# Kernel optimization log

Measured on AMD Instinct MI355X. Metric: run time of the kernel, lower is better.

The kernel has to match this reference:

```python
import jax, jax.numpy as jnp
import numpy as np

N_NODES = 8192
N_EDGES = 262144
D_IN = 512
D_OUT = 512


def setup_inputs() -> dict:
    key = jax.random.key(0)
    k1, k2, k3 = jax.random.split(key, 3)
    x = jax.random.normal(k1, (N_NODES, D_IN), dtype=jnp.float32)
    edge_index = jax.random.randint(k2, (2, N_EDGES), 0, N_NODES, dtype=jnp.int64)
    weight = jax.random.normal(k3, (D_IN, D_OUT), dtype=jnp.float32)
    bias = jnp.zeros((D_OUT,), dtype=jnp.float32)
    return {"x": x, "edge_index": edge_index, "weight": weight, "bias": bias}


def reference(x, edge_index, weight, bias):
    # GCN layer with selfloop=True branch of the original module.
    n = x.shape[0]
    # Dense symmetric adjacency via scatter-set, matching adj[ei0,ei1]=1; adj[ei1,ei0]=1
    adj = jnp.zeros((n, n), dtype=x.dtype)
    adj = adj.at[edge_index[0], edge_index[1]].set(1.0)
    adj = adj.at[edge_index[1], edge_index[0]].set(1.0)
    # Add self loops, symmetric degree normalization D^{-1/2} A D^{-1/2}
    adj = adj + jnp.eye(n, dtype=x.dtype)
    deg = jnp.sum(adj, axis=1)
    dinv = 1.0 / jnp.sqrt(deg)
    adj = adj * dinv[:, None] * dinv[None, :]  # == D @ adj @ D (diagonal scaling)
    return adj @ (x @ weight) + bias
```

## Files before the change

kernel.cpp:

```cpp
#include <hip/hip_runtime.h>
#include <hip/hip_bf16.h>


#define ELL_STRIDE 128

typedef __attribute__((ext_vector_type(8))) short bf16x8;
typedef __attribute__((ext_vector_type(4))) float f32x4;

__device__ __forceinline__ unsigned short f2bf(float f) {
  unsigned u = __float_as_uint(f);
  u = (u + 0x7fff + ((u >> 16) & 1)) >> 16;
  return (unsigned short)u;
}
__device__ __forceinline__ float bflo(unsigned u) {
  return __uint_as_float(u << 16);
}
__device__ __forceinline__ float bfhi(unsigned u) {
  return __uint_as_float(u & 0xffff0000u);
}

__global__ __launch_bounds__(256) void fused_front_kernel(
    const int* __restrict__ ei, unsigned* __restrict__ mask, int n_edges,
    int words,
    const float* __restrict__ x, unsigned short* __restrict__ xb, int n4,
    const float* __restrict__ W, unsigned short* __restrict__ Wt, int K, int N,
    unsigned short* __restrict__ Hs, int n_nodes,
    int edge_blocks, int cast_blocks, int tr_blocks) {
  const int bid = blockIdx.x;
  if (bid < edge_blocks) {
    const int e = bid * 256 + threadIdx.x;
    if (e < n_edges) {
      const int u = ei[e];
      const int v = ei[e + n_edges];
      atomicOr(&mask[(size_t)u * words + (v >> 5)], 1u << (v & 31));
      atomicOr(&mask[(size_t)v * words + (u >> 5)], 1u << (u & 31));
    }
    return;
  }
  if (bid < edge_blocks + cast_blocks) {
    const int t = (bid - edge_blocks) * 256 + threadIdx.x;
    if (t < n4) {
      float4 v = ((const float4*)x)[t];
      ushort4 o;
      o.x = f2bf(v.x); o.y = f2bf(v.y); o.z = f2bf(v.z); o.w = f2bf(v.w);
      ((ushort4*)xb)[t] = o;
    }
    return;
  }
  if (bid < edge_blocks + cast_blocks + tr_blocks) {
    __shared__ float tile[32][33];
    const int b = bid - edge_blocks - cast_blocks;
    const int bx = b & ((N >> 5) - 1);
    const int by = b >> (31 - __builtin_clz(N >> 5));
    const int tx = threadIdx.x & 31;
    const int ty = threadIdx.x >> 5;
#pragma unroll
    for (int r = 0; r < 4; ++r)
      tile[ty + 8 * r][tx] = W[(size_t)(by * 32 + ty + 8 * r) * N + bx * 32 + tx];
    __syncthreads();
#pragma unroll
    for (int r = 0; r < 4; ++r)
      Wt[(size_t)(bx * 32 + ty + 8 * r) * K + by * 32 + tx] =
          f2bf(tile[tx][ty + 8 * r]);
    return;
  }
  {
    const int t = threadIdx.x;
    if (t < (N >> 1)) ((unsigned*)(Hs + (size_t)n_nodes * N))[t] = 0;
  }
}

__global__ __launch_bounds__(256) void fused_mid_kernel(
    const unsigned short* __restrict__ xb,
    const unsigned short* __restrict__ Wt,
    unsigned short* __restrict__ Hs,
    const unsigned* __restrict__ mask, unsigned short* __restrict__ ell,
    int* __restrict__ deg, float* __restrict__ dinv,
    int M, int N, int K, int words, int gemm_blocks, int nbx_sh) {
  __shared__ unsigned short As[256 * 8];
  __shared__ unsigned short Bs[256 * 8];

  const int tid = threadIdx.x;
  const int bid = blockIdx.x;

  if (bid < gemm_blocks) {
    if (bid == 0 && tid == 0) dinv[M] = 0.f;
    const int wave = tid >> 6;
    const int lane = tid & 63;
    const int q = lane >> 4;
    const int c = lane & 15;
    const int bx = bid & ((1 << nbx_sh) - 1);
    const int by = bid >> nbx_sh;
    const int m0 = by * 64;
    const int n0 = bx * 64;
    const int wr = wave >> 1, wc = wave & 1;

    f32x4 acc[2][2] = {};

    for (int k0 = 0; k0 < K; k0 += 32) {
      {
        const unsigned short* g =
            xb + (size_t)(m0 + lane) * K + k0 + wave * 8;
        __builtin_amdgcn_global_load_lds(
            (const __attribute__((address_space(1))) void*)g,
            (__attribute__((address_space(3))) void*)(As + wave * 64 * 8), 16, 0, 0);
      }
      {
        const int s = tid;
        const unsigned short* g =
            Wt + (size_t)(n0 + (s >> 2)) * K + k0 + (s & 3) * 8;
        __builtin_amdgcn_global_load_lds(
            (const __attribute__((address_space(1))) void*)g,
            (__attribute__((address_space(3))) void*)(Bs + wave * 64 * 8), 16, 0, 0);
      }
      __syncthreads();

      bf16x8 a[2], b[2];
#pragma unroll
      for (int tm = 0; tm < 2; ++tm) {
        const int row = wr * 32 + tm * 16 + c;
        a[tm] = *(const bf16x8*)(As + (q * 64 + row) * 8);
      }
#pragma unroll
      for (int tn = 0; tn < 2; ++tn) {
        const int n = wc * 32 + tn * 16 + c;
        b[tn] = *(const bf16x8*)(Bs + (n * 4 + q) * 8);
      }
#pragma unroll
      for (int tm = 0; tm < 2; ++tm)
#pragma unroll
        for (int tn = 0; tn < 2; ++tn)
          acc[tm][tn] = __builtin_amdgcn_mfma_f32_16x16x32_bf16(
              a[tm], b[tn], acc[tm][tn], 0, 0, 0);
      __syncthreads();
    }

#pragma unroll
    for (int tm = 0; tm < 2; ++tm) {
#pragma unroll
      for (int r = 0; r < 4; ++r) {
        const int grow = m0 + wr * 32 + tm * 16 + q * 4 + r;
#pragma unroll
        for (int tn = 0; tn < 2; ++tn) {
          const int gcol = n0 + wc * 32 + tn * 16 + c;
          Hs[(size_t)grow * N + gcol] = f2bf(acc[tm][tn][r]);
        }
      }
    }
    return;
  }

  {
    const int wave = tid >> 6, lane = tid & 63;
    const int node = (bid - gemm_blocks) * 4 + wave;
    const unsigned* __restrict__ row = mask + (size_t)node * words;
    unsigned short* __restrict__ out = ell + (size_t)node * ELL_STRIDE;

    int running = 0;
    for (int r = 0; r < words; r += 64) {
      const int w = r + lane;
      unsigned bits = row[w];
      const int cnt = __popc(bits);
      int x = cnt;
#pragma unroll
      for (int d = 1; d < 64; d <<= 1) {
        int y = __shfl_up(x, d, 64);
        if (lane >= d) x += y;
      }
      int pos = running + x - cnt;
      while (bits) {
        const int b = __builtin_ctz(bits);
        bits &= bits - 1;
        if (pos < ELL_STRIDE) out[pos] = (unsigned short)((w << 5) + b);
        ++pos;
      }
      running += __shfl(x, 63, 64);
    }
    if (lane == 0) {
      const int dd = running < ELL_STRIDE ? running : ELL_STRIDE;
      deg[node] = dd;
      dinv[node] = rsqrtf((float)running + 1.0f);
      if (running < ELL_STRIDE) out[running] = (unsigned short)M;
      if (running + 1 < ELL_STRIDE) out[running + 1] = (unsigned short)M;
    }
  }
}

__global__ __launch_bounds__(256) void spmm_kernel(
    const unsigned short* __restrict__ ell, const int* __restrict__ deg,
    const float* __restrict__ dinv, const unsigned short* __restrict__ Hs,
    const float* __restrict__ bias, float* __restrict__ out, int n, int D) {
  __shared__ unsigned short jl[4][ELL_STRIDE];
  const int wave = threadIdx.x >> 6, lane = threadIdx.x & 63;
  const int i = blockIdx.x * 4 + wave;
  const int h = blockIdx.y;
  const int side = lane >> 5, hl = lane & 31;
  const int Dh = D >> 1;

  jl[wave][lane] = ell[(size_t)i * ELL_STRIDE + lane];
  jl[wave][64 + lane] = ell[(size_t)i * ELL_STRIDE + 64 + lane];
  const int d = deg[i];
  const float di = dinv[i];
  const int kmax = (d + 1) & ~1;

  const unsigned short* __restrict__ hb = Hs + h * Dh + hl * 8;
  float acc[8] = {0.f, 0.f, 0.f, 0.f, 0.f, 0.f, 0.f, 0.f};

  {
    const int js = side ? n : i;
    const float ds = side ? 0.f : di;
    const uint4 hv = *(const uint4*)(hb + (size_t)js * D);
    acc[0] += ds * bflo(hv.x); acc[1] += ds * bfhi(hv.x);
    acc[2] += ds * bflo(hv.y); acc[3] += ds * bfhi(hv.y);
    acc[4] += ds * bflo(hv.z); acc[5] += ds * bfhi(hv.z);
    acc[6] += ds * bflo(hv.w); acc[7] += ds * bfhi(hv.w);
  }
#pragma unroll 8
  for (int k = 0; k < kmax; k += 2) {
    const int j = jl[wave][k + side];
    const float dj = dinv[j];
    const uint4 hv = *(const uint4*)(hb + (size_t)j * D);
    acc[0] += dj * bflo(hv.x); acc[1] += dj * bfhi(hv.x);
    acc[2] += dj * bflo(hv.y); acc[3] += dj * bfhi(hv.y);
    acc[4] += dj * bflo(hv.z); acc[5] += dj * bfhi(hv.z);
    acc[6] += dj * bflo(hv.w); acc[7] += dj * bfhi(hv.w);
  }
#pragma unroll
  for (int t = 0; t < 8; ++t) acc[t] += __shfl_xor(acc[t], 32, 64);

  if (side == 0) {
    const float4 b0 = *(const float4*)(bias + h * Dh + hl * 8);
    const float4 b1 = *(const float4*)(bias + h * Dh + hl * 8 + 4);
    float* op = out + (size_t)i * D + h * Dh + hl * 8;
    float4 o0, o1;
    o0.x = di * acc[0] + b0.x; o0.y = di * acc[1] + b0.y;
    o0.z = di * acc[2] + b0.z; o0.w = di * acc[3] + b0.w;
    o1.x = di * acc[4] + b1.x; o1.y = di * acc[5] + b1.y;
    o1.z = di * acc[6] + b1.z; o1.w = di * acc[7] + b1.w;
    *(float4*)op = o0;
    *(float4*)(op + 4) = o1;
  }
}

extern "C" void kernel_launch(void* const* d_in, const int* in_sizes, int n_in,
                              void* d_out, int out_size, void* d_ws, size_t ws_size,
                              hipStream_t stream) {
  const float* x    = (const float*)d_in[0];
  const int*   ei   = (const int*)d_in[1];
  const float* W    = (const float*)d_in[2];
  const float* bias = (const float*)d_in[3];
  float* out = (float*)d_out;

  const int d_out_dim = in_sizes[3];
  const int d_in_dim  = in_sizes[2] / d_out_dim;
  const int n_nodes   = in_sizes[0] / d_in_dim;
  const int n_edges   = in_sizes[1] / 2;
  const int words     = (n_nodes + 31) / 32;

  char* ws = (char*)d_ws;
  size_t off = 0;
  unsigned* mask = (unsigned*)(ws + off); off += (size_t)n_nodes * words * 4;
  int* deg       = (int*)(ws + off);      off += (size_t)n_nodes * 4;
  float* dinv    = (float*)(ws + off);    off += (size_t)(n_nodes + 1) * 4;
  unsigned short* ell = (unsigned short*)(ws + off); off += (size_t)n_nodes * ELL_STRIDE * 2;
  unsigned short* xb  = (unsigned short*)(ws + off); off += (size_t)n_nodes * d_in_dim * 2;
  unsigned short* Wt  = (unsigned short*)(ws + off); off += (size_t)d_in_dim * d_out_dim * 2;
  unsigned short* Hs  = (unsigned short*)(ws + off);
  off += (size_t)(n_nodes + 1) * d_out_dim * 2;

  hipMemsetAsync(mask, 0, (size_t)n_nodes * words * 4, stream);

  const int edge_blocks = (n_edges + 255) / 256;
  const int n4 = n_nodes * d_in_dim / 4;
  const int cast_blocks = (n4 + 255) / 256;
  const int tr_blocks = (d_in_dim / 32) * (d_out_dim / 32);
  fused_front_kernel<<<edge_blocks + cast_blocks + tr_blocks + 1, 256, 0, stream>>>(
      ei, mask, n_edges, words, x, xb, n4, W, Wt, d_in_dim, d_out_dim,
      Hs, n_nodes, edge_blocks, cast_blocks, tr_blocks);

  const int nbx = d_out_dim / 64;
  const int nbx_sh = 31 - __builtin_clz(nbx);
  const int gemm_blocks = nbx * (n_nodes / 64);
  const int ell_blocks = n_nodes / 4;
  fused_mid_kernel<<<gemm_blocks + ell_blocks, 256, 0, stream>>>(
      xb, Wt, Hs, mask, ell, deg, dinv,
      n_nodes, d_out_dim, d_in_dim, words, gemm_blocks, nbx_sh);

  dim3 sgrid(n_nodes / 4, 2);
  spmm_kernel<<<sgrid, 256, 0, stream>>>(ell, deg, dinv, Hs, bias, out,
                                         n_nodes, d_out_dim);
}
```

Before: 161.0 us.

## Double GEMM K-step, fold self-loop into ELL, prefetch dinv into LDS

The GEMM loop now stages 64 K-elements per iteration instead of 32, so it runs half as many barrier pairs per tile, at the cost of twice the LDS footprint. The ELL builder writes the node itself as the self-loop entry and pads the rest of the row with the sentinel index. This removes the separate self-loop load in the SpMM. The SpMM also gathers dinv for every neighbour once into shared memory alongside the index, which takes the dependent global dinv load out of the inner loop. Zeroing of dinv[n] moves to the front kernel so the ELL and SpMM stages see it.

Measured after the change: 157.7 us (median of 2 runs). 2.0% less time.

```diff
diff --git a/kernel.cpp b/kernel.cpp
--- a/kernel.cpp
+++ b/kernel.cpp
@@ -24,7 +24,7 @@
     int words,
     const float* __restrict__ x, unsigned short* __restrict__ xb, int n4,
     const float* __restrict__ W, unsigned short* __restrict__ Wt, int K, int N,
-    unsigned short* __restrict__ Hs, int n_nodes,
+    unsigned short* __restrict__ Hs, float* __restrict__ dinv, int n_nodes,
     int edge_blocks, int cast_blocks, int tr_blocks) {
   const int bid = blockIdx.x;
   if (bid < edge_blocks) {
@@ -67,6 +67,7 @@
   {
     const int t = threadIdx.x;
     if (t < (N >> 1)) ((unsigned*)(Hs + (size_t)n_nodes * N))[t] = 0;
+    if (t == 0) dinv[n_nodes] = 0.f;
   }
 }
 
@@ -77,14 +78,13 @@
     const unsigned* __restrict__ mask, unsigned short* __restrict__ ell,
     int* __restrict__ deg, float* __restrict__ dinv,
     int M, int N, int K, int words, int gemm_blocks, int nbx_sh) {
-  __shared__ unsigned short As[256 * 8];
-  __shared__ unsigned short Bs[256 * 8];
+  __shared__ unsigned short As[512 * 8];
+  __shared__ unsigned short Bs[512 * 8];
 
   const int tid = threadIdx.x;
   const int bid = blockIdx.x;
 
   if (bid < gemm_blocks) {
-    if (bid == 0 && tid == 0) dinv[M] = 0.f;
     const int wave = tid >> 6;
     const int lane = tid & 63;
     const int q = lane >> 4;
@@ -97,41 +97,49 @@
 
     f32x4 acc[2][2] = {};
 
-    for (int k0 = 0; k0 < K; k0 += 32) {
-      {
+    for (int k0 = 0; k0 < K; k0 += 64) {
+#pragma unroll
+      for (int t = 0; t < 2; ++t) {
+        const int sbase = t * 256 + wave * 64;
+        const int s = sbase + lane;
         const unsigned short* g =
-            xb + (size_t)(m0 + lane) * K + k0 + wave * 8;
+            xb + (size_t)(m0 + (s & 63)) * K + k0 + (s >> 6) * 8;
         __builtin_amdgcn_global_load_lds(
             (const __attribute__((address_space(1))) void*)g,
-            (__attribute__((address_space(3))) void*)(As + wave * 64 * 8), 16, 0, 0);
-      }
-      {
-        const int s = tid;
+            (__attribute__((address_space(3))) void*)(As + sbase * 8), 16, 0, 0);
+      }
+#pragma unroll
+      for (int t = 0; t < 2; ++t) {
+        const int sbase = t * 256 + wave * 64;
+        const int s = sbase + lane;
         const unsigned short* g =
-            Wt + (size_t)(n0 + (s >> 2)) * K + k0 + (s & 3) * 8;
+            Wt + (size_t)(n0 + (s >> 3)) * K + k0 + (s & 7) * 8;
         __builtin_amdgcn_global_load_lds(
             (const __attribute__((address_space(1))) void*)g,
-            (__attribute__((address_space(3))) void*)(Bs + wave * 64 * 8), 16, 0, 0);
+            (__attribute__((address_space(3))) void*)(Bs + sbase * 8), 16, 0, 0);
       }
       __syncthreads();
 
-      bf16x8 a[2], b[2];
-#pragma unroll
-      for (int tm = 0; tm < 2; ++tm) {
-        const int row = wr * 32 + tm * 16 + c;
-        a[tm] = *(const bf16x8*)(As + (q * 64 + row) * 8);
-      }
-#pragma unroll
-      for (int tn = 0; tn < 2; ++tn) {
-        const int n = wc * 32 + tn * 16 + c;
-        b[tn] = *(const bf16x8*)(Bs + (n * 4 + q) * 8);
-      }
-#pragma unroll
-      for (int tm = 0; tm < 2; ++tm)
-#pragma unroll
-        for (int tn = 0; tn < 2; ++tn)
-          acc[tm][tn] = __builtin_amdgcn_mfma_f32_16x16x32_bf16(
-              a[tm], b[tn], acc[tm][tn], 0, 0, 0);
+#pragma unroll
+      for (int kk = 0; kk < 2; ++kk) {
+        bf16x8 a[2], b[2];
+#pragma unroll
+        for (int tm = 0; tm < 2; ++tm) {
+          const int row = wr * 32 + tm * 16 + c;
+          a[tm] = *(const bf16x8*)(As + (((kk * 4 + q) * 64) + row) * 8);
+        }
+#pragma unroll
+        for (int tn = 0; tn < 2; ++tn) {
+          const int n = wc * 32 + tn * 16 + c;
+          b[tn] = *(const bf16x8*)(Bs + (n * 8 + kk * 4 + q) * 8);
+        }
+#pragma unroll
+        for (int tm = 0; tm < 2; ++tm)
+#pragma unroll
+          for (int tn = 0; tn < 2; ++tn)
+            acc[tm][tn] = __builtin_amdgcn_mfma_f32_16x16x32_bf16(
+                a[tm], b[tn], acc[tm][tn], 0, 0, 0);
+      }
       __syncthreads();
     }
 
@@ -176,12 +184,12 @@
       }
       running += __shfl(x, 63, 64);
     }
+    for (int p = running + lane; p < ELL_STRIDE; p += 64)
+      out[p] = (unsigned short)(p == running ? node : M);
     if (lane == 0) {
-      const int dd = running < ELL_STRIDE ? running : ELL_STRIDE;
-      deg[node] = dd;
+      const int dd = running + 1;
+      deg[node] = dd < ELL_STRIDE ? dd : ELL_STRIDE;
       dinv[node] = rsqrtf((float)running + 1.0f);
-      if (running < ELL_STRIDE) out[running] = (unsigned short)M;
-      if (running + 1 < ELL_STRIDE) out[running + 1] = (unsigned short)M;
     }
   }
 }
@@ -190,15 +198,19 @@
     const unsigned short* __restrict__ ell, const int* __restrict__ deg,
     const float* __restrict__ dinv, const unsigned short* __restrict__ Hs,
     const float* __restrict__ bias, float* __restrict__ out, int n, int D) {
-  __shared__ unsigned short jl[4][ELL_STRIDE];
+  __shared__ uint2 ji[4][ELL_STRIDE];
   const int wave = threadIdx.x >> 6, lane = threadIdx.x & 63;
   const int i = blockIdx.x * 4 + wave;
   const int h = blockIdx.y;
   const int side = lane >> 5, hl = lane & 31;
   const int Dh = D >> 1;
 
-  jl[wave][lane] = ell[(size_t)i * ELL_STRIDE + lane];
-  jl[wave][64 + lane] = ell[(size_t)i * ELL_STRIDE + 64 + lane];
+  {
+    const unsigned j0 = ell[(size_t)i * ELL_STRIDE + lane];
+    const unsigned j1 = ell[(size_t)i * ELL_STRIDE + 64 + lane];
+    ji[wave][lane] = make_uint2(j0, __float_as_uint(dinv[j0]));
+    ji[wave][64 + lane] = make_uint2(j1, __float_as_uint(dinv[j1]));
+  }
   const int d = deg[i];
   const float di = dinv[i];
   const int kmax = (d + 1) & ~1;
@@ -206,19 +218,11 @@
   const unsigned short* __restrict__ hb = Hs + h * Dh + hl * 8;
   float acc[8] = {0.f, 0.f, 0.f, 0.f, 0.f, 0.f, 0.f, 0.f};
 
-  {
-    const int js = side ? n : i;
-    const float ds = side ? 0.f : di;
-    const uint4 hv = *(const uint4*)(hb + (size_t)js * D);
-    acc[0] += ds * bflo(hv.x); acc[1] += ds * bfhi(hv.x);
-    acc[2] += ds * bflo(hv.y); acc[3] += ds * bfhi(hv.y);
-    acc[4] += ds * bflo(hv.z); acc[5] += ds * bfhi(hv.z);
-    acc[6] += ds * bflo(hv.w); acc[7] += ds * bfhi(hv.w);
-  }
 #pragma unroll 8
   for (int k = 0; k < kmax; k += 2) {
-    const int j = jl[wave][k + side];
-    const float dj = dinv[j];
+    const uint2 e = ji[wave][k + side];
+    const int j = e.x;
+    const float dj = __uint_as_float(e.y);
     const uint4 hv = *(const uint4*)(hb + (size_t)j * D);
     acc[0] += dj * bflo(hv.x); acc[1] += dj * bfhi(hv.x);
     acc[2] += dj * bflo(hv.y); acc[3] += dj * bfhi(hv.y);
@@ -276,7 +280,7 @@
   const int tr_blocks = (d_in_dim / 32) * (d_out_dim / 32);
   fused_front_kernel<<<edge_blocks + cast_blocks + tr_blocks + 1, 256, 0, stream>>>(
       ei, mask, n_edges, words, x, xb, n4, W, Wt, d_in_dim, d_out_dim,
-      Hs, n_nodes, edge_blocks, cast_blocks, tr_blocks);
+      Hs, dinv, n_nodes, edge_blocks, cast_blocks, tr_blocks);
 
   const int nbx = d_out_dim / 64;
   const int nbx_sh = 31 - __builtin_clz(nbx);
```
